# Optimization experiments

Measured on AMD Instinct MI355X. Metric: run time of the kernel, lower is better.

Reference implementation:

```python
import jax, jax.numpy as jnp
import numpy as np

DT = 1.0
EPS = 1e-6


def setup_inputs() -> dict:
    key = jax.random.key(0)
    k1, k2, k3, k4 = jax.random.split(key, 4)
    batch, in_ch, out_ch, state_dim, T = 16, 256, 256, 256, 8192
    u = jax.random.normal(k1, (batch, in_ch, T), dtype=jnp.float32)
    raw_lambda = jax.random.normal(k2, (state_dim,), dtype=jnp.float32)
    B_c = jax.random.normal(k3, (in_ch, state_dim), dtype=jnp.float32) * (1.0 / in_ch ** 0.5)
    C = jax.random.normal(k4, (state_dim, out_ch), dtype=jnp.float32) * (1.0 / state_dim ** 0.5)
    return {"u": u, "raw_lambda": raw_lambda, "B_c": B_c, "C": C}


def reference(u, raw_lambda, B_c, C):
    # ZOH discretization of diagonal SSM (all-real here since raw_lambda is real)
    lam = -jax.nn.softplus(raw_lambda)                 # (N,)
    A_d = jnp.exp(lam * DT)                            # (N,)
    factor = jnp.where(jnp.abs(lam) > EPS, (A_d - 1.0) / lam, jnp.full_like(lam, DT))
    B_d = B_c * factor[None, :]                        # (in_ch, N)

    # Precompute driving inputs for every step in one big GEMM: (T, B, N)
    x = jnp.einsum('bct,cn->tbn', u, B_d)

    batch, state_dim = u.shape[0], raw_lambda.shape[0]

    def step(s, x_t):
        s = s * A_d[None, :] + x_t                     # diagonal recurrence
        return s, s

    s0 = jnp.zeros((batch, state_dim), dtype=u.dtype)
    _, states = jax.lax.scan(step, s0, x)              # states: (T, B, N)

    # Project all states at once: y (B, out_ch, T)
    y = jnp.einsum('tbn,no->bot', states, C)
    return y
```

## Files before the change

### kernel.cpp

```cpp
#include <hip/hip_runtime.h>
#include <math.h>

typedef __attribute__((ext_vector_type(8)))  short short8;
typedef __attribute__((ext_vector_type(16))) float f32x16;

#define B_  16
#define C_  256
#define N_  256
#define O_  256
#define T_  8192
#define L_  64
#define NC_ 128
#define XIMG 16896

#define GLL16(gptr, lptr) \
  __builtin_amdgcn_global_load_lds((const __attribute__((address_space(1))) void*)(gptr), \
                                   (__attribute__((address_space(3))) void*)(lptr), 16, 0, 0)

__device__ inline unsigned short f2bf(float x) {
    unsigned u = __float_as_uint(x);
    u += 0x7fff + ((u >> 16) & 1);
    return (unsigned short)(u >> 16);
}
__device__ inline float bf2f(unsigned short h) {
    return __uint_as_float(((unsigned)h) << 16);
}
__device__ inline f32x16 zero16() {
    f32x16 z;
    #pragma unroll
    for (int i = 0; i < 16; ++i) z[i] = 0.f;
    return z;
}

__global__ __launch_bounds__(256) void k_prep(
    const float* __restrict__ raw_lambda, const float* __restrict__ B_c,
    const float* __restrict__ Cmat,
    float* __restrict__ Ad, float* __restrict__ AL,
    unsigned short* __restrict__ BdKf, unsigned short* __restrict__ CKf)
{
    const int r = blockIdx.x;
    const int t = threadIdx.x;
    const int kk = r >> 5, ri = r & 31;
    const int s = ri >> 4, hi = (ri >> 3) & 1, j = ri & 7;
    const int nt = t >> 5, l = (hi << 5) | (t & 31);
    const int idx = (((kk * 8 + nt) * 2 + s) * 64 + l) * 8 + j;

    if (blockIdx.y == 0) {
        const float x  = raw_lambda[t];
        const float sp = (x > 20.f) ? x : log1pf(expf(x));
        const float lam = -sp;
        const float ad  = expf(lam);
        const float factor = (fabsf(lam) > 1e-6f) ? (ad - 1.f) / lam : 1.f;
        if (r == 0) {
            Ad[t] = ad;
            float al = ad;
            #pragma unroll
            for (int i = 0; i < 6; ++i) al *= al;
            AL[t] = al;
        }
        BdKf[idx] = f2bf(B_c[r * N_ + t] * factor);
    } else {
        CKf[idx] = f2bf(Cmat[r * O_ + t]);
    }
}

__global__ __launch_bounds__(256) void k_phaseA(
    const float* __restrict__ u, const unsigned short* __restrict__ BdKf,
    const float* __restrict__ Ad, float* __restrict__ p_last,
    unsigned short* __restrict__ X, int doX)
{
    __shared__ __align__(16) unsigned short xs[XIMG];
    __shared__ __align__(16) unsigned short ut[2][2688];
    __shared__ __align__(16) unsigned short bb[2][8192];

    const int k = blockIdx.x, b = blockIdx.y;
    const int tid = threadIdx.x;
    const int w = tid >> 6, l = tid & 63, lo = l & 31, hi = l >> 5;
    const int t0 = k * L_;
    const float* ub = u + (size_t)b * C_ * T_ + t0;

    auto load_u = [&](float4 v[2], int kk) {
        #pragma unroll
        for (int q = 0; q < 2; ++q) {
            const int i = q * 256 + tid, cl = i >> 4, t4 = i & 15;
            v[q] = *(const float4*)(ub + (size_t)(kk * 32 + cl) * T_ + t4 * 4);
        }
    };
    auto cvt_ut = [&](const float4 v[2], unsigned short* utb) {
        unsigned* ud = (unsigned*)utb;
        #pragma unroll
        for (int q = 0; q < 2; ++q) {
            const int i = q * 256 + tid, cl = i >> 4, t4 = i & 15;
            float4 a = v[q], p;
            p.x = __shfl_xor(a.x, 16); p.y = __shfl_xor(a.y, 16);
            p.z = __shfl_xor(a.z, 16); p.w = __shfl_xor(a.w, 16);
            const bool odd = (cl & 1) != 0;
            const float l0 = odd ? p.z : a.x, h0 = odd ? a.z : p.x;
            const float l1 = odd ? p.w : a.y, h1 = odd ? a.w : p.y;
            const int r0 = odd ? 2 : 0;
            ud[(4 * t4 + r0    ) * 21 + (cl >> 1)] = f2bf(l0) | ((unsigned)f2bf(h0) << 16);
            ud[(4 * t4 + r0 + 1) * 21 + (cl >> 1)] = f2bf(l1) | ((unsigned)f2bf(h1) << 16);
        }
    };
    auto stage_bb = [&](int kk, int buf) {
        const char* src = (const char*)(BdKf + kk * 8192);
        #pragma unroll
        for (int q = 0; q < 4; ++q)
            GLL16(src + q * 4096 + w * 1024 + (l << 4),
                  (char*)bb[buf] + q * 4096 + w * 1024);
    };

    f32x16 a00 = zero16(), a01 = zero16(), a10 = zero16(), a11 = zero16();
    float4 va[2], vb[2];

    load_u(va, 0);
    stage_bb(0, 0);
    cvt_ut(va, ut[0]);
    load_u(va, 1);
    __syncthreads();

    #pragma unroll
    for (int kk = 0; kk < 8; ++kk) {
        const int cur = kk & 1;
        if (kk < 7) stage_bb(kk + 1, cur ^ 1);
        if (kk < 6) { if (kk & 1) load_u(va, kk + 2); else load_u(vb, kk + 2); }
        #pragma unroll
        for (int s = 0; s < 2; ++s) {
            const short8 fa0 = *(const short8*)(ut[cur] + (lo     ) * 42 + s * 16 + hi * 8);
            const short8 fa1 = *(const short8*)(ut[cur] + (32 + lo) * 42 + s * 16 + hi * 8);
            const short8 fb0 = *(const short8*)(bb[cur] + (((2 * w + 0) * 2 + s) * 64 + l) * 8);
            const short8 fb1 = *(const short8*)(bb[cur] + (((2 * w + 1) * 2 + s) * 64 + l) * 8);
            a00 = __builtin_amdgcn_mfma_f32_32x32x16_bf16(fa0, fb0, a00, 0, 0, 0);
            a01 = __builtin_amdgcn_mfma_f32_32x32x16_bf16(fa0, fb1, a01, 0, 0, 0);
            a10 = __builtin_amdgcn_mfma_f32_32x32x16_bf16(fa1, fb0, a10, 0, 0, 0);
            a11 = __builtin_amdgcn_mfma_f32_32x32x16_bf16(fa1, fb1, a11, 0, 0, 0);
        }
        if (kk < 7) { if (kk & 1) cvt_ut(vb, ut[cur ^ 1]); else cvt_ut(va, ut[cur ^ 1]); }
        __syncthreads();
    }

    #pragma unroll
    for (int tt = 0; tt < 2; ++tt)
        #pragma unroll
        for (int q = 0; q < 2; ++q) {
            const f32x16 a = (tt == 0) ? (q == 0 ? a00 : a01) : (q == 0 ? a10 : a11);
            const int n = (2 * w + q) * 32 + lo;
            #pragma unroll
            for (int g = 0; g < 4; ++g)
                #pragma unroll
                for (int p = 0; p < 2; ++p)
                    *(unsigned*)(xs + n * 66 + tt * 32 + hi * 4 + g * 8 + p * 2)
                        = f2bf(a[g * 4 + 2 * p]) | ((unsigned)f2bf(a[g * 4 + 2 * p + 1]) << 16);
        }
    __syncthreads();

    {
        const float ad = Ad[tid];
        float s = 0.f;
        const unsigned* row = (const unsigned*)xs + tid * 33;
        #pragma unroll
        for (int m = 0; m < 32; ++m) {
            const unsigned dw = row[m];
            s = fmaf(s, ad, bf2f((unsigned short)(dw & 0xffff)));
            s = fmaf(s, ad, bf2f((unsigned short)(dw >> 16)));
        }
        p_last[((size_t)k * B_ + b) * N_ + tid] = s;
    }

    if (doX) {
        const int4* src = (const int4*)xs;
        int4* dst = (int4*)(X + ((size_t)k * B_ + b) * XIMG);
        #pragma unroll
        for (int q = 0; q < 8; ++q) dst[q * 256 + tid] = src[q * 256 + tid];
        if (tid < 64) dst[2048 + tid] = src[2048 + tid];
    }
}

__global__ __launch_bounds__(256) void k_phaseB(
    const float* __restrict__ p_last, const float* __restrict__ AL,
    float* __restrict__ carry)
{
    __shared__ float buf[32 * 256];
    const int b = blockIdx.x, n = threadIdx.x;
    const float al = AL[n];
    float cur = 0.f;
    for (int kc = 0; kc < 4; ++kc) {
        __syncthreads();
        #pragma unroll
        for (int q = 0; q < 32; ++q)
            buf[q * 256 + n] = p_last[((size_t)(kc * 32 + q) * B_ + b) * N_ + n];
        __syncthreads();
        #pragma unroll
        for (int q = 0; q < 32; ++q) {
            carry[((size_t)(kc * 32 + q) * B_ + b) * N_ + n] = cur;
            cur = fmaf(cur, al, buf[q * 256 + n]);
        }
    }
}

__global__ __launch_bounds__(256) void k_phaseC(
    const unsigned short* __restrict__ X, const unsigned short* __restrict__ CKf,
    const float* __restrict__ Ad, const float* __restrict__ carry,
    float* __restrict__ y)
{
    __shared__ __align__(16) unsigned short xs[XIMG];
    __shared__ __align__(16) unsigned short bb[2][8192];

    const int k = blockIdx.x, b = blockIdx.y;
    const int tid = threadIdx.x;
    const int w = tid >> 6, l = tid & 63, lo = l & 31, hi = l >> 5;
    const int t0 = k * L_;

    auto stage_bb = [&](int kk, int buf) {
        const char* src = (const char*)(CKf + kk * 8192);
        #pragma unroll
        for (int q = 0; q < 4; ++q)
            GLL16(src + q * 4096 + w * 1024 + (l << 4),
                  (char*)bb[buf] + q * 4096 + w * 1024);
    };

    stage_bb(0, 0);
    const float cv = carry[((size_t)k * B_ + b) * N_ + tid];
    {
        const char* src = (const char*)(X + ((size_t)k * B_ + b) * XIMG);
        #pragma unroll
        for (int q = 0; q < 8; ++q)
            GLL16(src + q * 4096 + w * 1024 + (l << 4),
                  (char*)xs + q * 4096 + w * 1024);
        if (w == 0) GLL16(src + 32768 + (l << 4), (char*)xs + 32768);
    }
    __syncthreads();

    float st[64];
    {
        const float ad = Ad[tid];
        float s = cv;
        const unsigned* row = (const unsigned*)xs + tid * 33;
        #pragma unroll
        for (int m = 0; m < 32; ++m) {
            const unsigned dw = row[m];
            s = fmaf(s, ad, bf2f((unsigned short)(dw & 0xffff)));  st[2 * m]     = s;
            s = fmaf(s, ad, bf2f((unsigned short)(dw >> 16)));     st[2 * m + 1] = s;
        }
    }
    __syncthreads();
    {
        const int nb = tid >> 3, nl = tid & 7;
        #pragma unroll
        for (int t = 0; t < 64; ++t)
            xs[t * 264 + (((nb ^ ((t >> 3) & 3)) << 3) | nl)] = f2bf(st[t]);
    }
    __syncthreads();

    f32x16 c00 = zero16(), c01 = zero16(), c10 = zero16(), c11 = zero16();
    #pragma unroll
    for (int kk = 0; kk < 8; ++kk) {
        const int cur = kk & 1;
        if (kk < 7) stage_bb(kk + 1, cur ^ 1);
        #pragma unroll
        for (int s = 0; s < 2; ++s) {
            short8 fa[2];
            #pragma unroll
            for (int tt = 0; tt < 2; ++tt) {
                const int t = tt * 32 + lo;
                const int blk = (kk * 4 + s * 2 + hi) ^ ((t >> 3) & 3);
                fa[tt] = *(const short8*)(xs + t * 264 + blk * 8);
            }
            const short8 fb0 = *(const short8*)(bb[cur] + (((2 * w + 0) * 2 + s) * 64 + l) * 8);
            const short8 fb1 = *(const short8*)(bb[cur] + (((2 * w + 1) * 2 + s) * 64 + l) * 8);
            c00 = __builtin_amdgcn_mfma_f32_32x32x16_bf16(fa[0], fb0, c00, 0, 0, 0);
            c01 = __builtin_amdgcn_mfma_f32_32x32x16_bf16(fa[0], fb1, c01, 0, 0, 0);
            c10 = __builtin_amdgcn_mfma_f32_32x32x16_bf16(fa[1], fb0, c10, 0, 0, 0);
            c11 = __builtin_amdgcn_mfma_f32_32x32x16_bf16(fa[1], fb1, c11, 0, 0, 0);
        }
        __syncthreads();
    }

    #pragma unroll
    for (int tt = 0; tt < 2; ++tt)
        #pragma unroll
        for (int q = 0; q < 2; ++q) {
            const f32x16 a = (tt == 0) ? (q == 0 ? c00 : c01) : (q == 0 ? c10 : c11);
            const int o = (2 * w + q) * 32 + lo;
            float* yo = y + ((size_t)b * O_ + o) * T_ + t0 + tt * 32 + hi * 4;
            #pragma unroll
            for (int g = 0; g < 4; ++g) {
                float4 v;
                v.x = a[g * 4 + 0]; v.y = a[g * 4 + 1];
                v.z = a[g * 4 + 2]; v.w = a[g * 4 + 3];
                *(float4*)(yo + g * 8) = v;
            }
        }
}

__device__ __forceinline__ void gemm1_rc(
    const float* __restrict__ u, const unsigned short* __restrict__ BdKf,
    int b, int k, unsigned short* xs, unsigned short* ut, unsigned short* bb)
{
    const int tid = threadIdx.x;
    const int w = tid >> 6, l = tid & 63, lo = l & 31, hi = l >> 5;
    const int t0 = k * L_;
    f32x16 a00 = zero16(), a01 = zero16(), a10 = zero16(), a11 = zero16();
    for (int kk = 0; kk < 8; ++kk) {
        #pragma unroll
        for (int q = 0; q < 2; ++q) {
            const int i = q * 256 + tid, cl = i >> 4, t4 = i & 15;
            const float4 v = *(const float4*)(
                u + ((size_t)b * C_ + kk * 32 + cl) * T_ + t0 + t4 * 4);
            ut[(t4 * 4 + 0) * 40 + cl] = f2bf(v.x);
            ut[(t4 * 4 + 1) * 40 + cl] = f2bf(v.y);
            ut[(t4 * 4 + 2) * 40 + cl] = f2bf(v.z);
            ut[(t4 * 4 + 3) * 40 + cl] = f2bf(v.w);
        }
        {
            const unsigned short* src = BdKf + kk * 8192;
            #pragma unroll
            for (int q = 0; q < 4; ++q) {
                const int i16 = q * 256 + tid;
                *(int4*)(bb + i16 * 8) = *(const int4*)(src + i16 * 8);
            }
        }
        __syncthreads();
        #pragma unroll
        for (int s = 0; s < 2; ++s) {
            const short8 fa0 = *(const short8*)(ut + (0 * 32 + lo) * 40 + s * 16 + hi * 8);
            const short8 fa1 = *(const short8*)(ut + (1 * 32 + lo) * 40 + s * 16 + hi * 8);
            const short8 fb0 = *(const short8*)(bb + (((2 * w + 0) * 2 + s) * 64 + l) * 8);
            const short8 fb1 = *(const short8*)(bb + (((2 * w + 1) * 2 + s) * 64 + l) * 8);
            a00 = __builtin_amdgcn_mfma_f32_32x32x16_bf16(fa0, fb0, a00, 0, 0, 0);
            a01 = __builtin_amdgcn_mfma_f32_32x32x16_bf16(fa0, fb1, a01, 0, 0, 0);
            a10 = __builtin_amdgcn_mfma_f32_32x32x16_bf16(fa1, fb0, a10, 0, 0, 0);
            a11 = __builtin_amdgcn_mfma_f32_32x32x16_bf16(fa1, fb1, a11, 0, 0, 0);
        }
        __syncthreads();
    }
    #pragma unroll
    for (int tt = 0; tt < 2; ++tt)
        #pragma unroll
        for (int q = 0; q < 2; ++q) {
            const f32x16 a = (tt == 0) ? (q == 0 ? a00 : a01) : (q == 0 ? a10 : a11);
            const int n = (2 * w + q) * 32 + lo;
            #pragma unroll
            for (int g = 0; g < 4; ++g)
                #pragma unroll
                for (int p = 0; p < 2; ++p)
                    *(unsigned*)(xs + n * 66 + tt * 32 + hi * 4 + g * 8 + p * 2)
                        = f2bf(a[g * 4 + 2 * p]) | ((unsigned)f2bf(a[g * 4 + 2 * p + 1]) << 16);
        }
    __syncthreads();
}

__global__ __launch_bounds__(256) void k_phaseC_rc(
    const float* __restrict__ u, const unsigned short* __restrict__ BdKf,
    const unsigned short* __restrict__ CKf, const float* __restrict__ Ad,
    const float* __restrict__ carry, float* __restrict__ y)
{
    __shared__ __align__(16) unsigned short xs[XIMG];
    __shared__ __align__(16) unsigned short ut[2560];
    __shared__ __align__(16) unsigned short bb[8192];

    const int k = blockIdx.x, b = blockIdx.y;
    const int tid = threadIdx.x;
    const int w = tid >> 6, l = tid & 63, lo = l & 31, hi = l >> 5;
    const int t0 = k * L_;

    gemm1_rc(u, BdKf, b, k, xs, ut, bb);

    {
        const float a = Ad[tid];
        float s = carry[((size_t)k * B_ + b) * N_ + tid];
        float st[64];
        #pragma unroll
        for (int m = 0; m < 32; ++m) {
            const unsigned dw = *(const unsigned*)(xs + tid * 66 + 2 * m);
            s = fmaf(s, a, bf2f((unsigned short)(dw & 0xffff)));  st[2 * m] = s;
            s = fmaf(s, a, bf2f((unsigned short)(dw >> 16)));     st[2 * m + 1] = s;
        }
        __syncthreads();
        #pragma unroll
        for (int t = 0; t < 64; ++t) xs[t * 264 + tid] = f2bf(st[t]);
    }
    __syncthreads();

    f32x16 c00 = zero16(), c01 = zero16(), c10 = zero16(), c11 = zero16();
    for (int kk = 0; kk < 8; ++kk) {
        __syncthreads();
        {
            const unsigned short* src = CKf + kk * 8192;
            #pragma unroll
            for (int q = 0; q < 4; ++q) {
                const int i16 = q * 256 + tid;
                *(int4*)(bb + i16 * 8) = *(const int4*)(src + i16 * 8);
            }
        }
        __syncthreads();
        #pragma unroll
        for (int s = 0; s < 2; ++s) {
            const short8 fa0 = *(const short8*)(xs + (0 * 32 + lo) * 264 + kk * 32 + s * 16 + hi * 8);
            const short8 fa1 = *(const short8*)(xs + (1 * 32 + lo) * 264 + kk * 32 + s * 16 + hi * 8);
            const short8 fb0 = *(const short8*)(bb + (((2 * w + 0) * 2 + s) * 64 + l) * 8);
            const short8 fb1 = *(const short8*)(bb + (((2 * w + 1) * 2 + s) * 64 + l) * 8);
            c00 = __builtin_amdgcn_mfma_f32_32x32x16_bf16(fa0, fb0, c00, 0, 0, 0);
            c01 = __builtin_amdgcn_mfma_f32_32x32x16_bf16(fa0, fb1, c01, 0, 0, 0);
            c10 = __builtin_amdgcn_mfma_f32_32x32x16_bf16(fa1, fb0, c10, 0, 0, 0);
            c11 = __builtin_amdgcn_mfma_f32_32x32x16_bf16(fa1, fb1, c11, 0, 0, 0);
        }
    }

    #pragma unroll
    for (int tt = 0; tt < 2; ++tt)
        #pragma unroll
        for (int q = 0; q < 2; ++q) {
            const f32x16 a = (tt == 0) ? (q == 0 ? c00 : c01) : (q == 0 ? c10 : c11);
            const int o = (2 * w + q) * 32 + lo;
            float* yo = y + ((size_t)b * O_ + o) * T_ + t0 + tt * 32 + hi * 4;
            #pragma unroll
            for (int g = 0; g < 4; ++g) {
                float4 v;
                v.x = a[g * 4 + 0]; v.y = a[g * 4 + 1];
                v.z = a[g * 4 + 2]; v.w = a[g * 4 + 3];
                *(float4*)(yo + g * 8) = v;
            }
        }
}

extern "C" void kernel_launch(void* const* d_in, const int* in_sizes, int n_in,
                              void* d_out, int out_size, void* d_ws, size_t ws_size,
                              hipStream_t stream)
{
    const float* u  = (const float*)d_in[0];
    const float* rl = (const float*)d_in[1];
    const float* Bc = (const float*)d_in[2];
    const float* Cm = (const float*)d_in[3];
    float* y  = (float*)d_out;
    char*  ws = (char*)d_ws;

    float* Ad     = (float*)(ws + 0);
    float* AL     = (float*)(ws + 1024);
    float* p_last = (float*)(ws + 2048);
    float* carry  = (float*)(ws + 2048 + 2097152);
    unsigned short* BdKf = (unsigned short*)(ws + 2048 + 2 * 2097152);
    unsigned short* CKf  = (unsigned short*)(ws + 2048 + 2 * 2097152 + 131072);
    unsigned short* X    = (unsigned short*)(ws + 2048 + 2 * 2097152 + 2 * 131072);
    const size_t need = 2048 + 2ull * 2097152 + 2ull * 131072
                      + (size_t)NC_ * B_ * XIMG * 2;
    const int doX = (ws_size >= need) ? 1 : 0;

    k_prep  <<<dim3(256, 2),  dim3(256), 0, stream>>>(rl, Bc, Cm, Ad, AL, BdKf, CKf);
    k_phaseA<<<dim3(NC_, B_), dim3(256), 0, stream>>>(u, BdKf, Ad, p_last, X, doX);
    k_phaseB<<<dim3(B_),      dim3(256), 0, stream>>>(p_last, AL, carry);
    if (doX)
        k_phaseC<<<dim3(NC_, B_), dim3(256), 0, stream>>>(X, CKf, Ad, carry, y);
    else
        k_phaseC_rc<<<dim3(NC_, B_), dim3(256), 0, stream>>>(u, BdKf, CKf, Ad, carry, y);
}
```

Baseline: 125.4 us.

## Store phase-A MFMA results to X directly in fragment layout, drop LDS staging

Phase A no longer writes the MFMA accumulators through a padded shared-memory image. It packs them to bf16 and writes them straight to global X in the MFMA fragment order. The chunk-end state is computed in registers with a Horner scheme over powers of A_d and combined across half-waves by shuffle. Phase C reads the new unpadded fragment layout from LDS into registers and runs the scan while writing swizzled states. This removes about 33KB of LDS, a barrier and padding traffic from phase A, at the cost of more complex indexing and a different floating-point summation order.

```diff
diff --git a/kernel.cpp b/kernel.cpp
--- a/kernel.cpp
+++ b/kernel.cpp
@@ -11,7 +11,6 @@
 #define T_  8192
 #define L_  64
 #define NC_ 128
-#define XIMG 16896
 
 #define GLL16(gptr, lptr) \
   __builtin_amdgcn_global_load_lds((const __attribute__((address_space(1))) void*)(gptr), \
@@ -69,7 +68,6 @@
     const float* __restrict__ Ad, float* __restrict__ p_last,
     unsigned short* __restrict__ X, int doX)
 {
-    __shared__ __align__(16) unsigned short xs[XIMG];
     __shared__ __align__(16) unsigned short ut[2][2688];
     __shared__ __align__(16) unsigned short bb[2][8192];
 
@@ -78,6 +76,9 @@
     const int w = tid >> 6, l = tid & 63, lo = l & 31, hi = l >> 5;
     const int t0 = k * L_;
     const float* ub = u + (size_t)b * C_ * T_ + t0;
+
+    const float adq0 = Ad[(2 * w + 0) * 32 + lo];
+    const float adq1 = Ad[(2 * w + 1) * 32 + lo];
 
     auto load_u = [&](float4 v[2], int kk) {
         #pragma unroll
@@ -139,40 +140,49 @@
         __syncthreads();
     }
 
-    #pragma unroll
-    for (int tt = 0; tt < 2; ++tt)
-        #pragma unroll
-        for (int q = 0; q < 2; ++q) {
-            const f32x16 a = (tt == 0) ? (q == 0 ? a00 : a01) : (q == 0 ? a10 : a11);
-            const int n = (2 * w + q) * 32 + lo;
-            #pragma unroll
-            for (int g = 0; g < 4; ++g)
+    if (doX) {
+        unsigned* Xd = (unsigned*)X + (size_t)(k * B_ + b) * 8192;
+        #pragma unroll
+        for (int f = 0; f < 4; ++f) {
+            const f32x16 a = (f == 0) ? a00 : (f == 1) ? a01 : (f == 2) ? a10 : a11;
+            unsigned dw[8];
+            #pragma unroll
+            for (int d = 0; d < 8; ++d)
+                dw[d] = f2bf(a[2 * d]) | ((unsigned)f2bf(a[2 * d + 1]) << 16);
+            unsigned* base = Xd + w * 2048 + f * 512 + l * 4;
+            *(int4*)(base)       = *(const int4*)&dw[0];
+            *(int4*)(base + 256) = *(const int4*)&dw[4];
+        }
+    }
+
+    {
+        float p[2];
+        #pragma unroll
+        for (int q = 0; q < 2; ++q) {
+            const float ad = q ? adq1 : adq0;
+            const float ad2 = ad * ad, ad4 = ad2 * ad2, ad8 = ad4 * ad4;
+            const float ad16 = ad8 * ad8, ad32 = ad16 * ad16;
+            float full[2];
+            #pragma unroll
+            for (int tt = 0; tt < 2; ++tt) {
+                const f32x16 a = (tt == 0) ? (q == 0 ? a00 : a01)
+                                           : (q == 0 ? a10 : a11);
+                float v[4];
                 #pragma unroll
-                for (int p = 0; p < 2; ++p)
-                    *(unsigned*)(xs + n * 66 + tt * 32 + hi * 4 + g * 8 + p * 2)
-                        = f2bf(a[g * 4 + 2 * p]) | ((unsigned)f2bf(a[g * 4 + 2 * p + 1]) << 16);
-        }
-    __syncthreads();
-
-    {
-        const float ad = Ad[tid];
-        float s = 0.f;
-        const unsigned* row = (const unsigned*)xs + tid * 33;
-        #pragma unroll
-        for (int m = 0; m < 32; ++m) {
-            const unsigned dw = row[m];
-            s = fmaf(s, ad, bf2f((unsigned short)(dw & 0xffff)));
-            s = fmaf(s, ad, bf2f((unsigned short)(dw >> 16)));
-        }
-        p_last[((size_t)k * B_ + b) * N_ + tid] = s;
-    }
-
-    if (doX) {
-        const int4* src = (const int4*)xs;
-        int4* dst = (int4*)(X + ((size_t)k * B_ + b) * XIMG);
-        #pragma unroll
-        for (int q = 0; q < 8; ++q) dst[q * 256 + tid] = src[q * 256 + tid];
-        if (tid < 64) dst[2048 + tid] = src[2048 + tid];
+                for (int g = 0; g < 4; ++g)
+                    v[g] = fmaf(fmaf(fmaf(a[4*g], ad, a[4*g+1]), ad, a[4*g+2]), ad, a[4*g+3]);
+                const float H = fmaf(fmaf(fmaf(v[0], ad8, v[1]), ad8, v[2]), ad8, v[3]);
+                float P = hi ? H : H * ad4;
+                P += __shfl_xor(P, 32);
+                full[tt] = P;
+            }
+            p[q] = fmaf(full[0], ad32, full[1]);
+        }
+        if (hi == 0) {
+            float* dst = p_last + (size_t)(k * B_ + b) * N_;
+            dst[(2 * w + 0) * 32 + lo] = p[0];
+            dst[(2 * w + 1) * 32 + lo] = p[1];
+        }
     }
 }
 
@@ -203,7 +213,7 @@
     const float* __restrict__ Ad, const float* __restrict__ carry,
     float* __restrict__ y)
 {
-    __shared__ __align__(16) unsigned short xs[XIMG];
+    __shared__ __align__(16) unsigned short xs[16896];
     __shared__ __align__(16) unsigned short bb[2][8192];
 
     const int k = blockIdx.x, b = blockIdx.y;
@@ -220,35 +230,55 @@
     };
 
     stage_bb(0, 0);
-    const float cv = carry[((size_t)k * B_ + b) * N_ + tid];
     {
-        const char* src = (const char*)(X + ((size_t)k * B_ + b) * XIMG);
+        const char* src = (const char*)X + (size_t)(k * B_ + b) * 32768;
         #pragma unroll
         for (int q = 0; q < 8; ++q)
             GLL16(src + q * 4096 + w * 1024 + (l << 4),
                   (char*)xs + q * 4096 + w * 1024);
-        if (w == 0) GLL16(src + 32768 + (l << 4), (char*)xs + 32768);
-    }
-    __syncthreads();
-
-    float st[64];
+    }
+    const float cv = carry[(size_t)(k * B_ + b) * N_ + tid];
+    const float ad = Ad[tid];
+    __syncthreads();
+
+    unsigned arr[2][2][8];
     {
-        const float ad = Ad[tid];
-        float s = cv;
-        const unsigned* row = (const unsigned*)xs + tid * 33;
-        #pragma unroll
-        for (int m = 0; m < 32; ++m) {
-            const unsigned dw = row[m];
-            s = fmaf(s, ad, bf2f((unsigned short)(dw & 0xffff)));  st[2 * m]     = s;
-            s = fmaf(s, ad, bf2f((unsigned short)(dw >> 16)));     st[2 * m + 1] = s;
-        }
-    }
-    __syncthreads();
+        const unsigned* xd = (const unsigned*)xs;
+        const int w2 = tid >> 6, q2 = (tid >> 5) & 1, lo2 = tid & 31;
+        #pragma unroll
+        for (int tt = 0; tt < 2; ++tt)
+            #pragma unroll
+            for (int h2 = 0; h2 < 2; ++h2) {
+                const unsigned* p = xd + w2 * 2048 + (tt * 2 + q2) * 512
+                                       + (h2 * 32 + lo2) * 4;
+                *(int4*)&arr[tt][h2][0] = *(const int4*)(p);
+                *(int4*)&arr[tt][h2][4] = *(const int4*)(p + 256);
+            }
+    }
+    __syncthreads();
+
     {
         const int nb = tid >> 3, nl = tid & 7;
-        #pragma unroll
-        for (int t = 0; t < 64; ++t)
-            xs[t * 264 + (((nb ^ ((t >> 3) & 3)) << 3) | nl)] = f2bf(st[t]);
+        float s = cv;
+        #pragma unroll
+        for (int tt = 0; tt < 2; ++tt)
+            #pragma unroll
+            for (int g = 0; g < 4; ++g)
+                #pragma unroll
+                for (int h2 = 0; h2 < 2; ++h2) {
+                    const unsigned d0 = arr[tt][h2][2 * g];
+                    const unsigned d1 = arr[tt][h2][2 * g + 1];
+                    const int tb = tt * 32 + 8 * g + 4 * h2;
+                    const int swz = (((nb ^ ((tb >> 3) & 3)) << 3) | nl);
+                    s = fmaf(s, ad, bf2f((unsigned short)(d0 & 0xffff)));
+                    xs[(tb + 0) * 264 + swz] = f2bf(s);
+                    s = fmaf(s, ad, bf2f((unsigned short)(d0 >> 16)));
+                    xs[(tb + 1) * 264 + swz] = f2bf(s);
+                    s = fmaf(s, ad, bf2f((unsigned short)(d1 & 0xffff)));
+                    xs[(tb + 2) * 264 + swz] = f2bf(s);
+                    s = fmaf(s, ad, bf2f((unsigned short)(d1 >> 16)));
+                    xs[(tb + 3) * 264 + swz] = f2bf(s);
+                }
     }
     __syncthreads();
 
@@ -355,7 +385,7 @@
     const unsigned short* __restrict__ CKf, const float* __restrict__ Ad,
     const float* __restrict__ carry, float* __restrict__ y)
 {
-    __shared__ __align__(16) unsigned short xs[XIMG];
+    __shared__ __align__(16) unsigned short xs[16896];
     __shared__ __align__(16) unsigned short ut[2560];
     __shared__ __align__(16) unsigned short bb[8192];
 
@@ -443,7 +473,7 @@
     unsigned short* CKf  = (unsigned short*)(ws + 2048 + 2 * 2097152 + 131072);
     unsigned short* X    = (unsigned short*)(ws + 2048 + 2 * 2097152 + 2 * 131072);
     const size_t need = 2048 + 2ull * 2097152 + 2ull * 131072
-                      + (size_t)NC_ * B_ * XIMG * 2;
+                      + (size_t)NC_ * B_ * 32768;
     const int doX = (ws_size >= need) ? 1 : 0;
 
     k_prep  <<<dim3(256, 2),  dim3(256), 0, stream>>>(rl, Bc, Cm, Ad, AL, BdKf, CKf);
```

Result: faster. 120.0 us (-4.3%).
